# Kernel tuning notes

Measured on AMD Instinct MI355X. Metric: run time of the kernel, lower is better.

The kernel has to match this reference:

```python
import jax, jax.numpy as jnp
import numpy as np

NUM_USERS = 100000
NUM_ITEMS = 200000
N = NUM_USERS + NUM_ITEMS
D = 64
NNZ = 5_000_000
B = 16384
N_LAYERS = 3


def setup_inputs() -> dict:
    key = jax.random.key(0)
    ks = jax.random.split(key, 7)
    users = jax.random.randint(ks[0], (B,), 0, NUM_USERS, dtype=jnp.int32)
    items = jax.random.randint(ks[1], (B,), 0, NUM_ITEMS, dtype=jnp.int32)
    edge_row = jax.random.randint(ks[2], (NNZ,), 0, N, dtype=jnp.int32)
    edge_col = jax.random.randint(ks[3], (NNZ,), 0, N, dtype=jnp.int32)
    # mimic D^-1/2 A D^-1/2 normalization scale (~1/avg_degree)
    edge_vals = jax.random.uniform(ks[4], (NNZ,), dtype=jnp.float32) * 0.06
    user_emb = jax.random.normal(ks[5], (NUM_USERS, D), dtype=jnp.float32) * 0.1
    item_emb = jax.random.normal(ks[6], (NUM_ITEMS, D), dtype=jnp.float32) * 0.1
    return {
        "users": users, "items": items,
        "edge_row": edge_row, "edge_col": edge_col, "edge_vals": edge_vals,
        "user_emb": user_emb, "item_emb": item_emb,
        "n_layers": N_LAYERS,
    }


def _spmm(edge_row, edge_col, edge_vals, x):
    # sparse [N,N] @ dense [N,D] via gather + segment_sum
    msg = x[edge_col] * edge_vals[:, None]  # [nnz, D]
    return jax.ops.segment_sum(msg, edge_row, num_segments=N)


def reference(users, items, edge_row, edge_col, edge_vals, user_emb, item_emb, n_layers):
    # LightGCN.computer(): propagate + mean over layers (running-sum form)
    all_emb = jnp.concatenate([user_emb, item_emb], axis=0)  # [N, D]
    acc = all_emb
    for _ in range(n_layers):
        all_emb = _spmm(edge_row, edge_col, edge_vals, all_emb)
        acc = acc + all_emb
    light_out = acc / (n_layers + 1)
    all_users = light_out[:NUM_USERS]
    all_items = light_out[NUM_USERS:]
    # forward(users, items): elementwise dot product
    users_emb = all_users[users]
    items_emb = all_items[items]
    gamma = jnp.sum(users_emb * items_emb, axis=1)  # [B]
    return gamma
```

## Files before the change

kernel.cpp:

```cpp
#include <hip/hip_runtime.h>
#include <hip/hip_fp16.h>
#include <hip/hip_fp8.h>

namespace {

constexpr int kUsers = 100000;
constexpr int kItems = 200000;
constexpr int kN     = kUsers + kItems;
constexpr int kD     = 64;
constexpr int kNNZ   = 5000000;
constexpr int kB     = 16384;
constexpr int kRowsPerBkt = 2048;
constexpr int kNBKT  = (kN + kRowsPerBkt - 1) / kRowsPerBkt;
constexpr int kSEPB  = 4096;
constexpr int kCE    = 8192;
constexpr int kMC    = 5;
constexpr int kCap   = kMC * kCE;
constexpr int kMaxSub = 2 * kB;

typedef int   v2i __attribute__((ext_vector_type(2)));
typedef float v4f __attribute__((ext_vector_type(4)));

#if defined(__has_builtin)
#if __has_builtin(__builtin_amdgcn_cvt_pk_f32_fp8) && __has_builtin(__builtin_amdgcn_cvt_f32_fp8)
#define NATIVE_FP8 1
#endif
#endif
#ifndef NATIVE_FP8
#define NATIVE_FP8 0
#endif

constexpr float kValScale = NATIVE_FP8 ? 1.0f : 256.0f;

__device__ inline void dec8(v2i h, float* f) {
#if NATIVE_FP8
  auto a0 = __builtin_amdgcn_cvt_pk_f32_fp8(h.x, false);
  auto a1 = __builtin_amdgcn_cvt_pk_f32_fp8(h.x, true);
  auto a2 = __builtin_amdgcn_cvt_pk_f32_fp8(h.y, false);
  auto a3 = __builtin_amdgcn_cvt_pk_f32_fp8(h.y, true);
  f[0] = a0[0]; f[1] = a0[1]; f[2] = a1[0]; f[3] = a1[1];
  f[4] = a2[0]; f[5] = a2[1]; f[6] = a3[0]; f[7] = a3[1];
#else
  unsigned int ws[2] = {(unsigned int)h.x, (unsigned int)h.y};
#pragma unroll
  for (int q = 0; q < 2; ++q) {
    unsigned int w = ws[q];
    unsigned int a = ((w & 0x007f007fu) << 7) | ((w & 0x00800080u) << 8);
    unsigned int b = (((w >> 8) & 0x007f007fu) << 7) | (((w >> 8) & 0x00800080u) << 8);
    float2 e = __half22float2(*reinterpret_cast<const __half2*>(&a));
    float2 o = __half22float2(*reinterpret_cast<const __half2*>(&b));
    f[4 * q + 0] = e.x; f[4 * q + 1] = o.x; f[4 * q + 2] = e.y; f[4 * q + 3] = o.y;
  }
#endif
}

__device__ inline float dec1(unsigned char b) {
#if NATIVE_FP8
  return __builtin_amdgcn_cvt_f32_fp8((int)b, 0) * 0.015625f;
#else
  unsigned int hb = ((b & 0x7fu) << 7) | ((b & 0x80u) << 8);
  return __half2float(__ushort_as_half((unsigned short)hb)) * 4.0f;
#endif
}

__device__ inline unsigned char enc(float f) { __hip_fp8_e4m3 q(f); return q.__x; }

__device__ inline float vdec(int w) {
  return __half2float(__ushort_as_half((unsigned short)((w >> 17) & 0x7FFC))) * kValScale;
}

__global__ void zero3(int* __restrict__ gpos, int* __restrict__ mark,
                      int* __restrict__ dh, int* __restrict__ scnt) {
  int i = blockIdx.x * blockDim.x + threadIdx.x;
  if (i < kN) mark[i] = 0;
  if (i < kNBKT + 1) gpos[i] = 0;
  if (i < 64) dh[i] = 0;
  if (i == 0) scnt[0] = 0;
}

__global__ void bucket_scatter(const int* __restrict__ row, const int* __restrict__ col,
                               const float* __restrict__ val, int* __restrict__ gpos,
                               int2* __restrict__ tmp) {
  __shared__ int hcnt[4][kNBKT];
  __shared__ int lofs[kNBKT];
  __shared__ int hbase[kNBKT];
  __shared__ int lds[256];
  __shared__ int2 se[kSEPB];
  __shared__ unsigned short sb[kSEPB];
  int t = threadIdx.x;
  int wv = t >> 6;
  long base = (long)blockIdx.x * kSEPB;
  int valid = (int)min((long)kSEPB, (long)kNNZ - base);
  for (int i = t; i < kNBKT; i += 256) {
    hcnt[0][i] = 0; hcnt[1][i] = 0; hcnt[2][i] = 0; hcnt[3][i] = 0;
  }
  __syncthreads();
  int pk[16], py[16], bk[16], rk[16];
  bool ok[16];
#pragma unroll
  for (int j = 0; j < 16; ++j) {
    long i = base + j * 256 + t;
    ok[j] = (i < kNNZ);
    if (ok[j]) {
      int r = __builtin_nontemporal_load(row + i);
      int c = __builtin_nontemporal_load(col + i);
      float v = __builtin_nontemporal_load(val + i);
      bk[j] = r >> 11;
      pk[j] = ((r & 2047) << 19) | c;
      unsigned short hb = __half_as_ushort(__float2half_rn(v));
      int v13 = ((int)hb + 2) >> 2;
      py[j] = c | (v13 << 19);
      rk[j] = atomicAdd(&hcnt[wv][bk[j]], 1);
    }
  }
  __syncthreads();
  int own = 0;
  if (t < kNBKT) {
    int c0 = hcnt[0][t], c1 = hcnt[1][t], c2 = hcnt[2][t], c3 = hcnt[3][t];
    hcnt[0][t] = 0; hcnt[1][t] = c0; hcnt[2][t] = c0 + c1; hcnt[3][t] = c0 + c1 + c2;
    own = c0 + c1 + c2 + c3;
  }
  lds[t] = own;
  __syncthreads();
  for (int o = 1; o < 256; o <<= 1) {
    int x = (t >= o) ? lds[t - o] : 0;
    __syncthreads();
    if (t >= o) lds[t] += x;
    __syncthreads();
  }
  if (t < kNBKT) {
    lofs[t] = lds[t] - own;
    hbase[t] = t * kCap + atomicAdd(&gpos[t], own);
  }
  __syncthreads();
#pragma unroll
  for (int j = 0; j < 16; ++j) {
    if (ok[j]) {
      int pos = lofs[bk[j]] + hcnt[wv][bk[j]] + rk[j];
      se[pos] = make_int2(pk[j], py[j]);
      sb[pos] = (unsigned short)bk[j];
    }
  }
  __syncthreads();
#pragma unroll
  for (int j = 0; j < 16; ++j) {
    int pos = t + j * 256;
    if (pos < valid) {
      int b = sb[pos];
      tmp[hbase[b] + (pos - lofs[b])] = se[pos];
    }
  }
}

__global__ void chunk_hist(const int* __restrict__ gpos, const int2* __restrict__ tmp,
                           int* __restrict__ ctab) {
  __shared__ int h[kRowsPerBkt];
  int b = blockIdx.x / kMC, c = blockIdx.x % kMC;
  int t = threadIdx.x;
  for (int i = t; i < kRowsPerBkt; i += 256) h[i] = 0;
  __syncthreads();
  int s = b * kCap + c * kCE;
  int e = b * kCap + gpos[b];
  if (s + kCE < e) e = s + kCE;
  for (int j = s + t; j < e; j += 256) atomicAdd(&h[tmp[j].x >> 19], 1);
  __syncthreads();
  int* dst = ctab + (size_t)blockIdx.x * kRowsPerBkt;
  for (int i = t; i < kRowsPerBkt; i += 256) dst[i] = h[i];
}

__global__ void scanA(int* __restrict__ ctab, int* __restrict__ rowptr,
                      int* __restrict__ partials) {
  __shared__ int lsum[256];
  int b = blockIdx.x, t = threadIdx.x;
  int cnt[8];
#pragma unroll
  for (int k = 0; k < 8; ++k) cnt[k] = 0;
  for (int c = 0; c < kMC; ++c) {
    int* p = ctab + (size_t)(b * kMC + c) * kRowsPerBkt;
#pragma unroll
    for (int k = 0; k < 8; ++k) {
      int idx = t * 8 + k;
      int v = p[idx];
      p[idx] = cnt[k];
      cnt[k] += v;
    }
  }
  int s = 0, pref[8];
#pragma unroll
  for (int k = 0; k < 8; ++k) { pref[k] = s; s += cnt[k]; }
  lsum[t] = s;
  __syncthreads();
  for (int o = 1; o < 256; o <<= 1) {
    int v = (t >= o) ? lsum[t - o] : 0;
    __syncthreads();
    if (t >= o) lsum[t] += v;
    __syncthreads();
  }
  int ex = (t == 0) ? 0 : lsum[t - 1];
#pragma unroll
  for (int k = 0; k < 8; ++k) {
    int r = b * kRowsPerBkt + t * 8 + k;
    if (r < kN) rowptr[r] = ex + pref[k];
  }
  if (t == 255) partials[b] = lsum[255];
}

__global__ void scan2(int* __restrict__ partials) {
  __shared__ int lds[256];
  int t = threadIdx.x;
  lds[t] = (t < kNBKT) ? partials[t] : 0;
  __syncthreads();
  for (int o = 1; o < 256; o <<= 1) {
    int v = (t >= o) ? lds[t - o] : 0;
    __syncthreads();
    if (t >= o) lds[t] += v;
    __syncthreads();
  }
  int ex = (t == 0) ? 0 : lds[t - 1];
  if (t < kNBKT) partials[t] = ex;
}

__global__ void scan3(int* __restrict__ rowptr, const int* __restrict__ partials) {
  int i = blockIdx.x * blockDim.x + threadIdx.x;
  if (i < kN) rowptr[i] += partials[i >> 11];
  else if (i == kN) rowptr[kN] = kNNZ;
}

__global__ void chunk_place(const int* __restrict__ gpos, const int2* __restrict__ tmp,
                            const int* __restrict__ rowptr, const int* __restrict__ ctab,
                            int* __restrict__ edges) {
  __shared__ int rank[kRowsPerBkt];
  int b = blockIdx.x / kMC, c = blockIdx.x % kMC;
  int t = threadIdx.x;
  for (int i = t; i < kRowsPerBkt; i += 256) rank[i] = 0;
  __syncthreads();
  int s = b * kCap + c * kCE;
  int e = b * kCap + gpos[b];
  if (s + kCE < e) e = s + kCE;
  const int* coff = ctab + (size_t)blockIdx.x * kRowsPerBkt;
  for (int j = s + t; j < e; j += 256) {
    int2 epk = tmp[j];
    int rl = epk.x >> 19;
    int k = atomicAdd(&rank[rl], 1);
    int dst = rowptr[b * kRowsPerBkt + rl] + coff[rl] + k;
    edges[dst] = epk.y;
  }
}

__global__ void mark_rows(const int* __restrict__ users, const int* __restrict__ items,
                          int* __restrict__ mark) {
  int i = blockIdx.x * blockDim.x + threadIdx.x;
  if (i >= kB) return;
  mark[users[i]] = 1;
  mark[kUsers + items[i]] = 1;
}

__global__ void sub_hist(const int* __restrict__ rowptr, const int* __restrict__ mark,
                         int* __restrict__ dh) {
  __shared__ int h[64];
  int t = threadIdx.x;
  if (t < 64) h[t] = 0;
  __syncthreads();
  int i = blockIdx.x * 256 + t;
  if (i < kN && mark[i]) {
    int d = min(rowptr[i + 1] - rowptr[i], 63);
    atomicAdd(&h[d], 1);
  }
  __syncthreads();
  if (t < 64 && h[t]) atomicAdd(&dh[t], h[t]);
}

__global__ void deg_scan(int* __restrict__ dh, int* __restrict__ scnt) {
  int t = threadIdx.x;
  int v = dh[t];
  int x = v;
  for (int o = 1; o < 64; o <<= 1) {
    int y = __shfl_up(x, o, 64);
    if (t >= o) x += y;
  }
  if (t == 63) *scnt = x;
  dh[t] = x - v;
}

__global__ void sub_place(const int* __restrict__ rowptr, const int* __restrict__ mark,
                          int* __restrict__ dh, int* __restrict__ list) {
  __shared__ int h[64], base[64];
  int t = threadIdx.x;
  if (t < 64) h[t] = 0;
  __syncthreads();
  int i = blockIdx.x * 256 + t;
  int d = 0, lr = 0;
  bool okv = (i < kN) && mark[i];
  if (okv) {
    d = min(rowptr[i + 1] - rowptr[i], 63);
    lr = atomicAdd(&h[d], 1);
  }
  __syncthreads();
  if (t < 64) base[t] = h[t] ? atomicAdd(&dh[t], h[t]) : 0;
  __syncthreads();
  if (okv) list[base[d] + lr] = i;
}

__global__ void mark_cols(const int* __restrict__ list, const int* __restrict__ cnt,
                          const int* __restrict__ rowptr, const int* __restrict__ edges,
                          int* __restrict__ mark) {
  int p = blockIdx.x * blockDim.x + threadIdx.x;
  if (p >= *cnt) return;
  int r = list[p];
  int s = rowptr[r], e = rowptr[r + 1];
  for (int j = s; j < e; ++j) mark[edges[j] & 0x7FFFF] = 1;
}

__global__ void to_fp8(const float* __restrict__ ue, const float* __restrict__ ie,
                       unsigned char* __restrict__ xq) {
  int t = blockIdx.x * blockDim.x + threadIdx.x;
  if (t >= kN * kD / 8) return;
  int row = t >> 3;
  int seg = t & 7;
  const float* src = (row < kUsers) ? (ue + (size_t)row * kD + seg * 8)
                                    : (ie + (size_t)(row - kUsers) * kD + seg * 8);
  v4f a = __builtin_nontemporal_load((const v4f*)src);
  v4f b = __builtin_nontemporal_load((const v4f*)src + 1);
  float f[8] = {a.x, a.y, a.z, a.w, b.x, b.y, b.z, b.w};
  unsigned int w0 = 0, w1 = 0;
#pragma unroll
  for (int k = 0; k < 4; ++k) w0 |= (unsigned int)enc(f[k] * 64.f) << (8 * k);
#pragma unroll
  for (int k = 0; k < 4; ++k) w1 |= (unsigned int)enc(f[4 + k] * 64.f) << (8 * k);
  v2i o; o.x = (int)w0; o.y = (int)w1;
  ((v2i*)xq)[t] = o;
}

template <int MODE>
__global__ __launch_bounds__(256, 8) void spmm(
    const int* __restrict__ rowptr, const int* __restrict__ edges,
    const unsigned char* __restrict__ x, unsigned char* __restrict__ yq,
    const int* __restrict__ aux, const int* __restrict__ cnt) {
  int t = threadIdx.x;
  int l = t & 7;
  int wid = (blockIdx.x * 256 + t) >> 6;
  int g = (t >> 3) & 7;
  int p = wid * 8 + g;
  int r = -1;
  bool live = false;
  if (MODE == 2) {
    int n = *cnt;
    if (p < n) { r = aux[p]; live = true; }
  } else {
    if (p < kN) { r = p; live = (MODE == 0) || (aux[r] != 0); }
  }
  int s = 0, e = 0;
  if (live) { s = rowptr[r]; e = rowptr[r + 1]; }
  int mx = e - s;
#pragma unroll
  for (int m = 8; m <= 32; m <<= 1) mx = max(mx, __shfl_xor(mx, m, 64));
  float acc[8];
#pragma unroll
  for (int k = 0; k < 8; ++k) acc[k] = 0.f;
  int last = max(e - 1, 0);
  int j = s;
  int E0 = edges[min(j, last)];
  int E1 = edges[min(j + 1, last)];
  int E2 = edges[min(j + 2, last)];
  int E3 = edges[min(j + 3, last)];
  for (int it = 0; it < mx; it += 4) {
    float v0 = (j     < e) ? vdec(E0) : 0.f;
    float v1 = (j + 1 < e) ? vdec(E1) : 0.f;
    float v2 = (j + 2 < e) ? vdec(E2) : 0.f;
    float v3 = (j + 3 < e) ? vdec(E3) : 0.f;
    v2i h0 = ((const v2i*)(x + (size_t)(E0 & 0x7FFFF) * kD))[l];
    v2i h1 = ((const v2i*)(x + (size_t)(E1 & 0x7FFFF) * kD))[l];
    v2i h2 = ((const v2i*)(x + (size_t)(E2 & 0x7FFFF) * kD))[l];
    v2i h3 = ((const v2i*)(x + (size_t)(E3 & 0x7FFFF) * kD))[l];
    j += 4;
    E0 = edges[min(j, last)];
    E1 = edges[min(j + 1, last)];
    E2 = edges[min(j + 2, last)];
    E3 = edges[min(j + 3, last)];
    float f[8];
    dec8(h0, f);
#pragma unroll
    for (int k = 0; k < 8; ++k) acc[k] = fmaf(v0, f[k], acc[k]);
    dec8(h1, f);
#pragma unroll
    for (int k = 0; k < 8; ++k) acc[k] = fmaf(v1, f[k], acc[k]);
    dec8(h2, f);
#pragma unroll
    for (int k = 0; k < 8; ++k) acc[k] = fmaf(v2, f[k], acc[k]);
    dec8(h3, f);
#pragma unroll
    for (int k = 0; k < 8; ++k) acc[k] = fmaf(v3, f[k], acc[k]);
  }
  if (live) {
    unsigned int w0 = 0, w1 = 0;
#pragma unroll
    for (int k = 0; k < 4; ++k) w0 |= (unsigned int)enc(acc[k]) << (8 * k);
#pragma unroll
    for (int k = 0; k < 4; ++k) w1 |= (unsigned int)enc(acc[4 + k]) << (8 * k);
    v2i o; o.x = (int)w0; o.y = (int)w1;
    ((v2i*)yq)[(size_t)r * 8 + l] = o;
  }
}

__global__ void acc_add_init(const int* __restrict__ users, const int* __restrict__ items,
                             const float* __restrict__ uemb, const float* __restrict__ iemb,
                             const unsigned char* __restrict__ xq, float* __restrict__ uacc,
                             float* __restrict__ iacc) {
  int tid = blockIdx.x * blockDim.x + threadIdx.x;
  if (tid >= kB * kD) return;
  int b = tid >> 6, d = tid & 63;
  int u = users[b], iw = items[b];
  uacc[tid] = uemb[(size_t)u * kD + d] + dec1(xq[(size_t)u * kD + d]);
  iacc[tid] = iemb[(size_t)iw * kD + d] + dec1(xq[(size_t)(kUsers + iw) * kD + d]);
}

__global__ void acc_add(const int* __restrict__ users, const int* __restrict__ items,
                        const unsigned char* __restrict__ xq, float* __restrict__ uacc,
                        float* __restrict__ iacc) {
  int tid = blockIdx.x * blockDim.x + threadIdx.x;
  if (tid >= kB * kD) return;
  int b = tid >> 6, d = tid & 63;
  uacc[tid] += dec1(xq[(size_t)users[b] * kD + d]);
  iacc[tid] += dec1(xq[(size_t)(kUsers + items[b]) * kD + d]);
}

__global__ void acc_add_fin(const int* __restrict__ users, const int* __restrict__ items,
                            const unsigned char* __restrict__ xq, const float* __restrict__ uacc,
                            const float* __restrict__ iacc, float* __restrict__ out) {
  int tid = blockIdx.x * blockDim.x + threadIdx.x;
  if (tid >= kB * kD) return;
  int b = tid >> 6, d = tid & 63;
  float u = uacc[tid] + dec1(xq[(size_t)users[b] * kD + d]);
  float v = iacc[tid] + dec1(xq[(size_t)(kUsers + items[b]) * kD + d]);
  float p = u * v;
  for (int o = 32; o > 0; o >>= 1) p += __shfl_down(p, o, 64);
  if (d == 0) out[b] = p * 0.0625f;
}

}

extern "C" void kernel_launch(void* const* d_in, const int* in_sizes, int n_in,
                              void* d_out, int out_size, void* d_ws, size_t ws_size,
                              hipStream_t stream) {
  const int*   users = (const int*)d_in[0];
  const int*   items = (const int*)d_in[1];
  const int*   erow  = (const int*)d_in[2];
  const int*   ecol  = (const int*)d_in[3];
  const float* evals = (const float*)d_in[4];
  const float* uemb  = (const float*)d_in[5];
  const float* iemb  = (const float*)d_in[6];
  float* out = (float*)d_out;

  char* ws = (char*)d_ws;
  size_t off = 0;
  auto take = [&](size_t bytes) -> char* {
    char* p = ws + off;
    off = (off + bytes + 255) & ~(size_t)255;
    return p;
  };
  int*    rowptr   = (int*)take((size_t)(kN + 1) * 4);
  int*    gpos     = (int*)take((kNBKT + 1) * 4);
  int*    partials = (int*)take(256 * 4);
  int*    dh       = (int*)take(256 * 4);
  int*    mark     = (int*)take((size_t)kN * 4);
  int*    list     = (int*)take((size_t)kMaxSub * 4);
  int*    scnt     = (int*)take(256);
  int*    edges    = (int*)take((size_t)kNNZ * 4);
  int2*   tmp      = (int2*)take((size_t)kNBKT * kCap * 8);
  unsigned char* xq0 = (unsigned char*)take((size_t)kN * kD);
  unsigned char* xq1 = (unsigned char*)take((size_t)kN * kD);
  float*  uacc     = (float*)take((size_t)kB * kD * 4);
  float*  iacc     = (float*)take((size_t)kB * kD * 4);
  int*    ctab     = (int*)xq0;
  (void)ws_size; (void)in_sizes; (void)n_in; (void)out_size;

  const int nScatBlocks = (kNNZ + kSEPB - 1) / kSEPB;
  const int nSpmmBlocks = (kN + 31) / 32;
  const int nSubBlocks  = (kMaxSub + 31) / 32;
  const int nRowBlocks  = (kN + 255) / 256;

  zero3<<<nRowBlocks, 256, 0, stream>>>(gpos, mark, dh, scnt);
  bucket_scatter<<<nScatBlocks, 256, 0, stream>>>(erow, ecol, evals, gpos, tmp);
  chunk_hist<<<kNBKT * kMC, 256, 0, stream>>>(gpos, tmp, ctab);
  scanA<<<kNBKT, 256, 0, stream>>>(ctab, rowptr, partials);
  scan2<<<1, 256, 0, stream>>>(partials);
  scan3<<<(kN + 1 + 255) / 256, 256, 0, stream>>>(rowptr, partials);
  chunk_place<<<kNBKT * kMC, 256, 0, stream>>>(gpos, tmp, rowptr, ctab, edges);

  mark_rows<<<(kB + 255) / 256, 256, 0, stream>>>(users, items, mark);
  sub_hist<<<nRowBlocks, 256, 0, stream>>>(rowptr, mark, dh);
  deg_scan<<<1, 64, 0, stream>>>(dh, scnt);
  sub_place<<<nRowBlocks, 256, 0, stream>>>(rowptr, mark, dh, list);
  mark_cols<<<(kMaxSub + 255) / 256, 256, 0, stream>>>(list, scnt, rowptr, edges, mark);

  to_fp8<<<(kN * kD / 8 + 255) / 256, 256, 0, stream>>>(uemb, iemb, xq0);
  spmm<0><<<nSpmmBlocks, 256, 0, stream>>>(rowptr, edges, xq0, xq1, nullptr, nullptr);
  acc_add_init<<<(kB * kD) / 256, 256, 0, stream>>>(users, items, uemb, iemb, xq1, uacc, iacc);
  spmm<1><<<nSpmmBlocks, 256, 0, stream>>>(rowptr, edges, xq1, xq0, mark, nullptr);
  acc_add<<<(kB * kD) / 256, 256, 0, stream>>>(users, items, xq0, uacc, iacc);
  spmm<2><<<nSubBlocks, 256, 0, stream>>>(rowptr, edges, xq0, xq1, list, scnt);
  acc_add_fin<<<(kB * kD) / 256, 256, 0, stream>>>(users, items, xq1, uacc, iacc, out);
}
```

Baseline: 521.5 us.

## Replace per-chunk histogram CSR build with global row counters and atomic placement

```diff
diff --git a/kernel.cpp b/kernel.cpp
--- a/kernel.cpp
+++ b/kernel.cpp
@@ -69,10 +69,11 @@
   return __half2float(__ushort_as_half((unsigned short)((w >> 17) & 0x7FFC))) * kValScale;
 }
 
-__global__ void zero3(int* __restrict__ gpos, int* __restrict__ mark,
-                      int* __restrict__ dh, int* __restrict__ scnt) {
+__global__ void zero4(int* __restrict__ gpos, int* __restrict__ mark,
+                      int* __restrict__ rowcnt, int* __restrict__ dh,
+                      int* __restrict__ scnt) {
   int i = blockIdx.x * blockDim.x + threadIdx.x;
-  if (i < kN) mark[i] = 0;
+  if (i < kN) { mark[i] = 0; rowcnt[i] = 0; }
   if (i < kNBKT + 1) gpos[i] = 0;
   if (i < 64) dh[i] = 0;
   if (i == 0) scnt[0] = 0;
@@ -80,12 +81,14 @@
 
 __global__ void bucket_scatter(const int* __restrict__ row, const int* __restrict__ col,
                                const float* __restrict__ val, int* __restrict__ gpos,
-                               int2* __restrict__ tmp) {
+                               int* __restrict__ rowcnt, int* __restrict__ tmp4,
+                               unsigned short* __restrict__ tmpr) {
   __shared__ int hcnt[4][kNBKT];
   __shared__ int lofs[kNBKT];
   __shared__ int hbase[kNBKT];
   __shared__ int lds[256];
-  __shared__ int2 se[kSEPB];
+  __shared__ int sp[kSEPB];
+  __shared__ unsigned short sr[kSEPB];
   __shared__ unsigned short sb[kSEPB];
   int t = threadIdx.x;
   int wv = t >> 6;
@@ -95,7 +98,7 @@
     hcnt[0][i] = 0; hcnt[1][i] = 0; hcnt[2][i] = 0; hcnt[3][i] = 0;
   }
   __syncthreads();
-  int pk[16], py[16], bk[16], rk[16];
+  int py[16], bk[16], rl[16], rk[16];
   bool ok[16];
 #pragma unroll
   for (int j = 0; j < 16; ++j) {
@@ -106,11 +109,12 @@
       int c = __builtin_nontemporal_load(col + i);
       float v = __builtin_nontemporal_load(val + i);
       bk[j] = r >> 11;
-      pk[j] = ((r & 2047) << 19) | c;
+      rl[j] = r & 2047;
       unsigned short hb = __half_as_ushort(__float2half_rn(v));
       int v13 = ((int)hb + 2) >> 2;
       py[j] = c | (v13 << 19);
       rk[j] = atomicAdd(&hcnt[wv][bk[j]], 1);
+      atomicAdd(&rowcnt[r], 1);
     }
   }
   __syncthreads();
@@ -137,7 +141,8 @@
   for (int j = 0; j < 16; ++j) {
     if (ok[j]) {
       int pos = lofs[bk[j]] + hcnt[wv][bk[j]] + rk[j];
-      se[pos] = make_int2(pk[j], py[j]);
+      sp[pos] = py[j];
+      sr[pos] = (unsigned short)rl[j];
       sb[pos] = (unsigned short)bk[j];
     }
   }
@@ -147,43 +152,22 @@
     int pos = t + j * 256;
     if (pos < valid) {
       int b = sb[pos];
-      tmp[hbase[b] + (pos - lofs[b])] = se[pos];
+      int w = hbase[b] + (pos - lofs[b]);
+      tmp4[w] = sp[pos];
+      tmpr[w] = sr[pos];
     }
   }
 }
 
-__global__ void chunk_hist(const int* __restrict__ gpos, const int2* __restrict__ tmp,
-                           int* __restrict__ ctab) {
-  __shared__ int h[kRowsPerBkt];
-  int b = blockIdx.x / kMC, c = blockIdx.x % kMC;
-  int t = threadIdx.x;
-  for (int i = t; i < kRowsPerBkt; i += 256) h[i] = 0;
-  __syncthreads();
-  int s = b * kCap + c * kCE;
-  int e = b * kCap + gpos[b];
-  if (s + kCE < e) e = s + kCE;
-  for (int j = s + t; j < e; j += 256) atomicAdd(&h[tmp[j].x >> 19], 1);
-  __syncthreads();
-  int* dst = ctab + (size_t)blockIdx.x * kRowsPerBkt;
-  for (int i = t; i < kRowsPerBkt; i += 256) dst[i] = h[i];
-}
-
-__global__ void scanA(int* __restrict__ ctab, int* __restrict__ rowptr,
+__global__ void scanR(const int* __restrict__ rowcnt, int* __restrict__ rowptr,
                       int* __restrict__ partials) {
   __shared__ int lsum[256];
   int b = blockIdx.x, t = threadIdx.x;
   int cnt[8];
 #pragma unroll
-  for (int k = 0; k < 8; ++k) cnt[k] = 0;
-  for (int c = 0; c < kMC; ++c) {
-    int* p = ctab + (size_t)(b * kMC + c) * kRowsPerBkt;
-#pragma unroll
-    for (int k = 0; k < 8; ++k) {
-      int idx = t * 8 + k;
-      int v = p[idx];
-      p[idx] = cnt[k];
-      cnt[k] += v;
-    }
+  for (int k = 0; k < 8; ++k) {
+    int idx = b * kRowsPerBkt + t * 8 + k;
+    cnt[k] = (idx < kN) ? rowcnt[idx] : 0;
   }
   int s = 0, pref[8];
 #pragma unroll
@@ -220,30 +204,31 @@
   if (t < kNBKT) partials[t] = ex;
 }
 
-__global__ void scan3(int* __restrict__ rowptr, const int* __restrict__ partials) {
+__global__ void scan3(int* __restrict__ rowptr, const int* __restrict__ partials,
+                      int* __restrict__ rowcur) {
   int i = blockIdx.x * blockDim.x + threadIdx.x;
-  if (i < kN) rowptr[i] += partials[i >> 11];
-  else if (i == kN) rowptr[kN] = kNNZ;
-}
-
-__global__ void chunk_place(const int* __restrict__ gpos, const int2* __restrict__ tmp,
-                            const int* __restrict__ rowptr, const int* __restrict__ ctab,
-                            int* __restrict__ edges) {
-  __shared__ int rank[kRowsPerBkt];
+  if (i < kN) {
+    int v = rowptr[i] + partials[i >> 11];
+    rowptr[i] = v;
+    rowcur[i] = v;
+  } else if (i == kN) {
+    rowptr[kN] = kNNZ;
+  }
+}
+
+__global__ void place(const int* __restrict__ gpos, const int* __restrict__ tmp4,
+                      const unsigned short* __restrict__ tmpr,
+                      int* __restrict__ rowcur, int* __restrict__ edges) {
   int b = blockIdx.x / kMC, c = blockIdx.x % kMC;
   int t = threadIdx.x;
-  for (int i = t; i < kRowsPerBkt; i += 256) rank[i] = 0;
-  __syncthreads();
   int s = b * kCap + c * kCE;
   int e = b * kCap + gpos[b];
   if (s + kCE < e) e = s + kCE;
-  const int* coff = ctab + (size_t)blockIdx.x * kRowsPerBkt;
   for (int j = s + t; j < e; j += 256) {
-    int2 epk = tmp[j];
-    int rl = epk.x >> 19;
-    int k = atomicAdd(&rank[rl], 1);
-    int dst = rowptr[b * kRowsPerBkt + rl] + coff[rl] + k;
-    edges[dst] = epk.y;
+    int pay = tmp4[j];
+    int r = b * kRowsPerBkt + (int)tmpr[j];
+    int dst = atomicAdd(&rowcur[r], 1);
+    edges[dst] = pay;
   }
 }
 
@@ -463,15 +448,17 @@
   int*    partials = (int*)take(256 * 4);
   int*    dh       = (int*)take(256 * 4);
   int*    mark     = (int*)take((size_t)kN * 4);
+  int*    rowcnt   = (int*)take((size_t)kN * 4);
   int*    list     = (int*)take((size_t)kMaxSub * 4);
   int*    scnt     = (int*)take(256);
   int*    edges    = (int*)take((size_t)kNNZ * 4);
-  int2*   tmp      = (int2*)take((size_t)kNBKT * kCap * 8);
+  int*    tmp4     = (int*)take((size_t)kNBKT * kCap * 4);
+  unsigned short* tmpr = (unsigned short*)take((size_t)kNBKT * kCap * 2);
   unsigned char* xq0 = (unsigned char*)take((size_t)kN * kD);
   unsigned char* xq1 = (unsigned char*)take((size_t)kN * kD);
   float*  uacc     = (float*)take((size_t)kB * kD * 4);
   float*  iacc     = (float*)take((size_t)kB * kD * 4);
-  int*    ctab     = (int*)xq0;
+  int*    rowcur   = rowcnt;
   (void)ws_size; (void)in_sizes; (void)n_in; (void)out_size;
 
   const int nScatBlocks = (kNNZ + kSEPB - 1) / kSEPB;
@@ -479,13 +466,13 @@
   const int nSubBlocks  = (kMaxSub + 31) / 32;
   const int nRowBlocks  = (kN + 255) / 256;
 
-  zero3<<<nRowBlocks, 256, 0, stream>>>(gpos, mark, dh, scnt);
-  bucket_scatter<<<nScatBlocks, 256, 0, stream>>>(erow, ecol, evals, gpos, tmp);
-  chunk_hist<<<kNBKT * kMC, 256, 0, stream>>>(gpos, tmp, ctab);
-  scanA<<<kNBKT, 256, 0, stream>>>(ctab, rowptr, partials);
+  zero4<<<nRowBlocks, 256, 0, stream>>>(gpos, mark, rowcnt, dh, scnt);
+  bucket_scatter<<<nScatBlocks, 256, 0, stream>>>(erow, ecol, evals, gpos, rowcnt,
+                                                  tmp4, tmpr);
+  scanR<<<kNBKT, 256, 0, stream>>>(rowcnt, rowptr, partials);
   scan2<<<1, 256, 0, stream>>>(partials);
-  scan3<<<(kN + 1 + 255) / 256, 256, 0, stream>>>(rowptr, partials);
-  chunk_place<<<kNBKT * kMC, 256, 0, stream>>>(gpos, tmp, rowptr, ctab, edges);
+  scan3<<<(kN + 1 + 255) / 256, 256, 0, stream>>>(rowptr, partials, rowcur);
+  place<<<kNBKT * kMC, 256, 0, stream>>>(gpos, tmp4, tmpr, rowcur, edges);
 
   mark_rows<<<(kB + 255) / 256, 256, 0, stream>>>(users, items, mark);
   sub_hist<<<nRowBlocks, 256, 0, stream>>>(rowptr, mark, dh);
```

Measured after the change: 953.4 us. 1.83x slower.
